# Kernel tuning notes

Measured on AMD Instinct MI355X. Metric: run time of the kernel, lower is better.

## Reference

```python
import jax, jax.numpy as jnp
import numpy as np

B, R, E, H = 1024, 1024, 1024, 512
L_ATTR, L_OBJ, L_RELA = 16, 36, 64
EPS = 1e-8


def _lstm_cell(x, h, c, Wih, Whh, bih, bhh):
    # torch.nn.LSTMCell: gates ordered i, f, g, o
    g = x @ Wih.T + bih + h @ Whh.T + bhh
    i, f, gg, o = jnp.split(g, 4, axis=1)
    c2 = jax.nn.sigmoid(f) * c + jax.nn.sigmoid(i) * jnp.tanh(gg)
    h2 = jax.nn.sigmoid(o) * jnp.tanh(c2)
    return h2, c2


def _attend(h, feats, p_feats, mask, Wq, bq, wa, ba):
    att_h = h @ Wq.T + bq                         # [B,H]
    dot = jnp.tanh(p_feats + att_h[:, None, :])   # [B,L,H]
    scores = dot @ wa + ba                        # [B,L]
    w = jax.nn.softmax(scores, axis=1)
    w = w * mask
    w = w / (w.sum(1, keepdims=True) + EPS)
    return jnp.einsum('bl,bld->bd', w, feats)     # [B,R]


def setup_inputs() -> dict:
    key = jax.random.key(0)
    ks = iter(jax.random.split(key, 64))
    n = lambda shp, s=0.02: jax.random.normal(next(ks), shp, dtype=jnp.float32) * s
    inp = {
        'xt': n((B, E), 1.0), 'fc_feats': n((B, R), 1.0),
        'state_h': n((2, B, R), 1.0), 'state_c': n((2, B, R), 1.0),
        'attr_feats': n((B, L_ATTR, R), 1.0), 'obj_feats': n((B, L_OBJ, R), 1.0),
        'rela_feats': n((B, L_RELA, R), 1.0),
        'p_attr_feats': n((B, L_ATTR, H), 1.0), 'p_obj_feats': n((B, L_OBJ, H), 1.0),
        'p_rela_feats': n((B, L_RELA, H), 1.0),
        'attr_masks': jnp.ones((B, L_ATTR), jnp.float32),
        'att_masks': jnp.ones((B, L_OBJ), jnp.float32),
        'rela_masks': jnp.ones((B, L_RELA), jnp.float32),
        'att_Wih': n((4 * R, E + 2 * R)), 'att_Whh': n((4 * R, R)),
        'att_bih': n((4 * R,)), 'att_bhh': n((4 * R,)),
        'lang_Wih': n((4 * R, 4 * R)), 'lang_Whh': n((4 * R, R)),
        'lang_bih': n((4 * R,)), 'lang_bhh': n((4 * R,)),
    }
    for p in ('attr', 'obj', 'rela'):
        inp[p + '_Wq'] = n((H, R)); inp[p + '_bq'] = n((H,))
        inp[p + '_wa'] = n((H,));   inp[p + '_ba'] = n((1,))
    return inp


def reference(xt, fc_feats, state_h, state_c, attr_feats, obj_feats, rela_feats,
              p_attr_feats, p_obj_feats, p_rela_feats, attr_masks, att_masks,
              rela_masks, att_Wih, att_Whh, att_bih, att_bhh, lang_Wih, lang_Whh,
              lang_bih, lang_bhh, attr_Wq, attr_bq, attr_wa, attr_ba, obj_Wq,
              obj_bq, obj_wa, obj_ba, rela_Wq, rela_bq, rela_wa, rela_ba):
    prev_h = state_h[-1]
    att_in = jnp.concatenate([prev_h, fc_feats, xt], axis=1)
    h_att, c_att = _lstm_cell(att_in, state_h[0], state_c[0],
                              att_Wih, att_Whh, att_bih, att_bhh)
    a_attr = _attend(h_att, attr_feats, p_attr_feats, attr_masks,
                     attr_Wq, attr_bq, attr_wa, attr_ba)
    a_obj = _attend(h_att, obj_feats, p_obj_feats, att_masks,
                    obj_Wq, obj_bq, obj_wa, obj_ba)
    a_rela = _attend(h_att, rela_feats, p_rela_feats, rela_masks,
                     rela_Wq, rela_bq, rela_wa, rela_ba)
    lang_in = jnp.concatenate([h_att, a_attr, a_obj, a_rela], axis=1)
    h_lang, c_lang = _lstm_cell(lang_in, state_h[1], state_c[1],
                                lang_Wih, lang_Whh, lang_bih, lang_bhh)
    # dropout in eval mode -> identity
    output = h_lang
    return output, jnp.stack([h_att, h_lang]), jnp.stack([c_att, c_lang])
```

## Files before the change

kernel.cpp:

```cpp
#include <hip/hip_runtime.h>
#include <math.h>

typedef _Float16 half8  __attribute__((ext_vector_type(8)));
typedef _Float16 half4v __attribute__((ext_vector_type(4)));
typedef float    f32x4  __attribute__((ext_vector_type(4)));

__device__ __forceinline__ _Float16 f2h(float f) { return (_Float16)f; }

__device__ __forceinline__ float tanh_fast(float x) {
    float e = __expf(2.f * x);
    return 1.f - 2.f / (e + 1.f);
}

#define LDSB (128 * 40)

__device__ __forceinline__ void gemm_body(
    _Float16* __restrict__ sm,
    const float* A0, const float* A1, const float* A2p, const float* A3,
    const float* A4,
    const float* W0, const float* W1, const float* W2,
    int w0cols, int w0s, int w1s, int nsel,
    _Float16* __restrict__ Cpart, int ldc,
    int kb, int kLen, int ntile, int mtile, int zout)
{
    _Float16* smA = sm;
    _Float16* smW = sm + 2 * LDSB;
    const int tid  = threadIdx.x;
    const int lane = tid & 63;
    const int wid  = tid >> 6;
    const int wm   = wid >> 1, wn = wid & 1;
    const int m0   = mtile * 128;
    const int n0   = ntile * 128;
    const int nt   = kLen >> 5;
    const int srow = tid >> 3;
    const int scol = (tid & 7) << 2;
    const int fr   = lane & 15;
    const int kq   = lane >> 4;

    const float* wsel = nullptr;
    if (nsel) {
        int sel = n0 >> 9;
        const float* Wq = (sel == 0) ? W0 : (sel == 1) ? W1 : W2;
        wsel = Wq + (size_t)((n0 & 511) + srow) * 1024 + kb + scol;
    }

    f32x4 acc[4][4] = {};
    float4 va[4], vw[4];

    auto LOADA = [&](int lk) {
        int gk = kb + lk;
        int seg = gk >> 10;
        const float* ap = (seg == 0) ? A0 : (seg == 1) ? A1 : (seg == 2) ? A2p
                        : (seg == 3) ? A3 : A4;
        ap += (size_t)(m0 + srow) * 1024 + (gk & 1023) + scol;
        #pragma unroll
        for (int p = 0; p < 4; ++p)
            va[p] = *reinterpret_cast<const float4*>(ap + (size_t)p * 32 * 1024);
    };
    auto LOADW = [&](int lk) {
        const float* wp; int wstr;
        if (nsel) {
            wp = wsel + lk; wstr = 1024;
        } else {
            int gk = kb + lk;
            if (gk < w0cols) { wp = W0 + (size_t)(n0 + srow) * w0s + gk + scol;            wstr = w0s; }
            else             { wp = W1 + (size_t)(n0 + srow) * w1s + (gk - w0cols) + scol; wstr = w1s; }
        }
        #pragma unroll
        for (int p = 0; p < 4; ++p)
            vw[p] = *reinterpret_cast<const float4*>(wp + (size_t)p * 32 * wstr);
    };
    auto WRITEA = [&](int buf) {
        _Float16* d = smA + buf * LDSB;
        #pragma unroll
        for (int p = 0; p < 4; ++p) {
            half4v h = { f2h(va[p].x), f2h(va[p].y), f2h(va[p].z), f2h(va[p].w) };
            *reinterpret_cast<half4v*>(&d[(srow + p * 32) * 40 + scol]) = h;
        }
    };
    auto WRITEW = [&](int buf) {
        _Float16* d = smW + buf * LDSB;
        #pragma unroll
        for (int p = 0; p < 4; ++p) {
            half4v h = { f2h(vw[p].x), f2h(vw[p].y), f2h(vw[p].z), f2h(vw[p].w) };
            *reinterpret_cast<half4v*>(&d[(srow + p * 32) * 40 + scol]) = h;
        }
    };
    auto DOMFMA = [&](int buf) {
        half8 af[4], bf[4];
        _Float16* sA = smA + buf * LDSB;
        _Float16* sW = smW + buf * LDSB;
        #pragma unroll
        for (int i = 0; i < 4; ++i) {
            af[i] = *reinterpret_cast<const half8*>(&sA[(wm * 64 + i * 16 + fr) * 40 + kq * 8]);
            bf[i] = *reinterpret_cast<const half8*>(&sW[(wn * 64 + i * 16 + fr) * 40 + kq * 8]);
        }
        #pragma unroll
        for (int i = 0; i < 4; ++i)
            #pragma unroll
            for (int j = 0; j < 4; ++j)
                acc[i][j] = __builtin_amdgcn_mfma_f32_16x16x32_f16(af[i], bf[j], acc[i][j], 0, 0, 0);
    };

    LOADA(0); LOADW(0);
    WRITEA(0); WRITEW(0);
    __syncthreads();
    int cur = 0;
    for (int it = 0; it < nt - 1; ++it) {
        LOADA((it + 1) * 32);
        LOADW((it + 1) * 32);
        DOMFMA(cur);
        WRITEA(cur ^ 1);
        WRITEW(cur ^ 1);
        __syncthreads();
        cur ^= 1;
    }
    DOMFMA(cur);

    _Float16* cp = Cpart + (size_t)zout * 1024ull * (size_t)ldc;
    #pragma unroll
    for (int j = 0; j < 4; ++j) {
        int nc = n0 + wn * 64 + j * 16 + fr;
        #pragma unroll
        for (int i = 0; i < 4; ++i) {
            int rb = m0 + wm * 64 + i * 16 + kq * 4;
            #pragma unroll
            for (int r = 0; r < 4; ++r)
                cp[(size_t)(rb + r) * ldc + nc] = (_Float16)acc[i][j][r];
        }
    }
}

__global__ __launch_bounds__(256) void gemm_hf(
    const float* A0, const float* A1, const float* A2p, const float* A3,
    const float* A4,
    const float* W0, const float* W1, const float* W2,
    int w0cols, int w0s, int w1s, int nsel,
    _Float16* Cpart, int ldc, int kLen, int zbase)
{
    __shared__ _Float16 sm[4 * LDSB];
    gemm_body(sm, A0, A1, A2p, A3, A4, W0, W1, W2, w0cols, w0s, w1s, nsel,
              Cpart, ldc, blockIdx.z * kLen, kLen,
              blockIdx.x, blockIdx.y, zbase + blockIdx.z);
}

__global__ __launch_bounds__(256) void gemm_hf_swz(
    const float* A0, const float* A1, const float* A2p, const float* A3,
    const float* A4,
    const float* W0, const float* W1, const float* W2,
    int w0cols, int w0s, int w1s,
    _Float16* Cpart, int ldc, int kLen, int zsplit)
{
    __shared__ _Float16 sm[4 * LDSB];
    const int bid = blockIdx.x;
    const int xcd = bid & 7;
    const int j   = bid >> 3;
    const int grp = xcd * (zsplit * 4) + (j >> 3);
    const int mtile = j & 7;
    const int ntile = grp / zsplit;
    const int z     = grp % zsplit;
    gemm_body(sm, A0, A1, A2p, A3, A4, W0, W1, W2, w0cols, w0s, w1s, 0,
              Cpart, ldc, z * kLen, kLen, ntile, mtile, z);
}


__global__ __launch_bounds__(256) void att_scores(
    const float* __restrict__ p_attr, const float* __restrict__ p_obj,
    const float* __restrict__ p_rela,
    const _Float16* __restrict__ q16,
    const float* __restrict__ attr_bq, const float* __restrict__ obj_bq,
    const float* __restrict__ rela_bq,
    const float* __restrict__ attr_wa, const float* __restrict__ obj_wa,
    const float* __restrict__ rela_wa,
    const float* __restrict__ attr_ba, const float* __restrict__ obj_ba,
    const float* __restrict__ rela_ba,
    float* __restrict__ scg)
{
    const unsigned gw = blockIdx.x * 4u + (threadIdx.x >> 6);
    const int lane = threadIdx.x & 63;
    const unsigned b = gw / 116u;
    const int r = (int)(gw - b * 116u);
    const float* pf; const float* bq; const float* wa; const float* ba;
    int l, moff, scoff, L;
    if (r < 16)      { pf = p_attr; bq = attr_bq; wa = attr_wa; ba = attr_ba; l = r;      moff = 0;    scoff = 0;  L = 16; }
    else if (r < 52) { pf = p_obj;  bq = obj_bq;  wa = obj_wa;  ba = obj_ba;  l = r - 16; moff = 512;  scoff = 16; L = 36; }
    else             { pf = p_rela; bq = rela_bq; wa = rela_wa; ba = rela_ba; l = r - 52; moff = 1024; scoff = 52; L = 64; }

    const float4* pf4 = reinterpret_cast<const float4*>(pf) + ((size_t)b * L + l) * 128 + lane * 2;
    float4 a0 = pf4[0];
    float4 a1 = pf4[1];
    const _Float16* qb = q16 + (size_t)b * 1536 + moff + lane * 8;
    half8 hq0 = *reinterpret_cast<const half8*>(qb);
    half8 hq1 = *reinterpret_cast<const half8*>(qb + 1536ull * 1024);
    const float4* bq4 = reinterpret_cast<const float4*>(bq) + lane * 2;
    const float4* wa4 = reinterpret_cast<const float4*>(wa) + lane * 2;
    float4 b0 = bq4[0], b1 = bq4[1];
    float4 w0 = wa4[0], w1 = wa4[1];

    float s = tanh_fast(a0.x + (float)hq0[0] + (float)hq1[0] + b0.x) * w0.x
            + tanh_fast(a0.y + (float)hq0[1] + (float)hq1[1] + b0.y) * w0.y
            + tanh_fast(a0.z + (float)hq0[2] + (float)hq1[2] + b0.z) * w0.z
            + tanh_fast(a0.w + (float)hq0[3] + (float)hq1[3] + b0.w) * w0.w
            + tanh_fast(a1.x + (float)hq0[4] + (float)hq1[4] + b1.x) * w1.x
            + tanh_fast(a1.y + (float)hq0[5] + (float)hq1[5] + b1.y) * w1.y
            + tanh_fast(a1.z + (float)hq0[6] + (float)hq1[6] + b1.z) * w1.z
            + tanh_fast(a1.w + (float)hq0[7] + (float)hq1[7] + b1.w) * w1.w;
    #pragma unroll
    for (int off = 32; off >= 1; off >>= 1) s += __shfl_xor(s, off);
    if (lane == 0) scg[(size_t)b * 128 + scoff + l] = s + ba[0];
}

template<int L>
__device__ __forceinline__ void wsum_mod(
    const float* __restrict__ feats, const float* __restrict__ scg_b,
    const float* __restrict__ mask_b,
    float* __restrict__ outa, int b, float* wgt)
{
    const int tid = threadIdx.x;
    if (tid < 64) {
        float v = (tid < L) ? scg_b[tid] : -1e30f;
        float m = v;
        #pragma unroll
        for (int off = 32; off >= 1; off >>= 1) m = fmaxf(m, __shfl_xor(m, off));
        float e = (tid < L) ? __expf(v - m) : 0.f;
        float sum = e;
        #pragma unroll
        for (int off = 32; off >= 1; off >>= 1) sum += __shfl_xor(sum, off);
        float w = e / sum;
        float wm = (tid < L) ? w * mask_b[tid] : 0.f;
        float s2 = wm;
        #pragma unroll
        for (int off = 32; off >= 1; off >>= 1) s2 += __shfl_xor(s2, off);
        wgt[tid] = wm / (s2 + 1e-8f);
    }
    __syncthreads();

    const int d0 = tid * 4;
    const float* fp = feats + (size_t)b * L * 1024 + d0;
    f32x4 acc = {0.f, 0.f, 0.f, 0.f};
    constexpr int NFULL = L / 8;
    float4 vA[8], vB[8];
    #pragma unroll
    for (int j = 0; j < 8; ++j)
        vA[j] = *reinterpret_cast<const float4*>(fp + (size_t)j * 1024);
    #pragma unroll
    for (int g = 0; g < NFULL; ++g) {
        float4* cur = (g & 1) ? vB : vA;
        float4* nxt = (g & 1) ? vA : vB;
        if (g + 1 < NFULL) {
            #pragma unroll
            for (int j = 0; j < 8; ++j)
                nxt[j] = *reinterpret_cast<const float4*>(fp + (size_t)((g + 1) * 8 + j) * 1024);
        }
        #pragma unroll
        for (int j = 0; j < 8; ++j) {
            const float w = wgt[g * 8 + j];
            acc[0] += w * cur[j].x; acc[1] += w * cur[j].y;
            acc[2] += w * cur[j].z; acc[3] += w * cur[j].w;
        }
    }
    #pragma unroll
    for (int lg = NFULL * 8; lg < L; ++lg) {
        float4 v = *reinterpret_cast<const float4*>(fp + (size_t)lg * 1024);
        const float w = wgt[lg];
        acc[0] += w * v.x; acc[1] += w * v.y; acc[2] += w * v.z; acc[3] += w * v.w;
    }
    float4 o; o.x = acc[0]; o.y = acc[1]; o.z = acc[2]; o.w = acc[3];
    *reinterpret_cast<float4*>(outa + (size_t)b * 1024 + d0) = o;
}

__global__ __launch_bounds__(256) void att_wsum(
    const float* __restrict__ attr_feats, const float* __restrict__ obj_feats,
    const float* __restrict__ rela_feats,
    const float* __restrict__ attr_masks, const float* __restrict__ att_masks,
    const float* __restrict__ rela_masks,
    const float* __restrict__ scg,
    float* __restrict__ a32)
{
    __shared__ float wgt[64];
    const int bid = blockIdx.x;
    const int mod = bid % 3;
    const int b   = bid / 3;
    if (mod == 0)
        wsum_mod<16>(attr_feats, scg + (size_t)b * 128 + 0,  attr_masks + (size_t)b * 16,
                     a32, b, wgt);
    else if (mod == 1)
        wsum_mod<36>(obj_feats,  scg + (size_t)b * 128 + 16, att_masks + (size_t)b * 36,
                     a32 + 1024ull * 1024, b, wgt);
    else
        wsum_mod<64>(rela_feats, scg + (size_t)b * 128 + 52, rela_masks + (size_t)b * 64,
                     a32 + 2ull * 1024 * 1024, b, wgt);
}

__global__ __launch_bounds__(256) void lstm4(
    const _Float16* __restrict__ g, size_t zstride, int nz,
    const float* __restrict__ bih, const float* __restrict__ bhh,
    const float* __restrict__ c_prev,
    float* __restrict__ hA, float* __restrict__ hB,
    float* __restrict__ c_out)
{
    int idx = blockIdx.x * 256 + threadIdx.x;
    int b = idx >> 10, r = idx & 1023;
    size_t base = (size_t)b * 4096;
    float gi = bih[r]        + bhh[r];
    float gf = bih[1024 + r] + bhh[1024 + r];
    float gg = bih[2048 + r] + bhh[2048 + r];
    float go = bih[3072 + r] + bhh[3072 + r];
    for (int z = 0; z < nz; ++z) {
        const _Float16* gz = g + (size_t)z * zstride + base;
        gi += (float)gz[r];
        gf += (float)gz[1024 + r];
        gg += (float)gz[2048 + r];
        go += (float)gz[3072 + r];
    }
    float si = 1.f / (1.f + __expf(-gi));
    float sf = 1.f / (1.f + __expf(-gf));
    float so = 1.f / (1.f + __expf(-go));
    float c2 = sf * c_prev[idx] + si * tanh_fast(gg);
    float h2 = so * tanh_fast(c2);
    hA[idx] = h2;
    if (hB) hB[idx] = h2;
    c_out[idx] = c2;
}

extern "C" void kernel_launch(void* const* d_in, const int* in_sizes, int n_in,
                              void* d_out, int out_size, void* d_ws, size_t ws_size,
                              hipStream_t stream)
{
    const size_t BR = 1024ull * 1024ull;
    const float* xt         = (const float*)d_in[0];
    const float* fc         = (const float*)d_in[1];
    const float* state_h    = (const float*)d_in[2];
    const float* state_c    = (const float*)d_in[3];
    const float* attr_feats = (const float*)d_in[4];
    const float* obj_feats  = (const float*)d_in[5];
    const float* rela_feats = (const float*)d_in[6];
    const float* p_attr     = (const float*)d_in[7];
    const float* p_obj      = (const float*)d_in[8];
    const float* p_rela     = (const float*)d_in[9];
    const float* attr_masks = (const float*)d_in[10];
    const float* att_masks  = (const float*)d_in[11];
    const float* rela_masks = (const float*)d_in[12];
    const float* att_Wih    = (const float*)d_in[13];
    const float* att_Whh    = (const float*)d_in[14];
    const float* att_bih    = (const float*)d_in[15];
    const float* att_bhh    = (const float*)d_in[16];
    const float* lang_Wih   = (const float*)d_in[17];
    const float* lang_Whh   = (const float*)d_in[18];
    const float* lang_bih   = (const float*)d_in[19];
    const float* lang_bhh   = (const float*)d_in[20];
    const float* attr_Wq    = (const float*)d_in[21];
    const float* attr_bq    = (const float*)d_in[22];
    const float* attr_wa    = (const float*)d_in[23];
    const float* attr_ba    = (const float*)d_in[24];
    const float* obj_Wq     = (const float*)d_in[25];
    const float* obj_bq     = (const float*)d_in[26];
    const float* obj_wa     = (const float*)d_in[27];
    const float* obj_ba     = (const float*)d_in[28];
    const float* rela_Wq    = (const float*)d_in[29];
    const float* rela_bq    = (const float*)d_in[30];
    const float* rela_wa    = (const float*)d_in[31];
    const float* rela_ba    = (const float*)d_in[32];

    float* out = (float*)d_out;
    const float* h0 = state_h;
    const float* h1 = state_h + BR;
    float* h_att = out + BR;
    float* scg  = out;

    const bool big = ws_size >= 52428800ull;
    const int gslots = big ? 4 : 2;
    _Float16* g16 = (_Float16*)d_ws;
    _Float16* q16 = g16 + (size_t)gslots * 4ull * BR;
    float*    a32 = (float*)(q16 + 2ull * 1536 * 1024);
    float* a_attr = a32;
    float* a_obj  = a32 + BR;
    float* a_rela = a32 + 2 * BR;

    dim3 blk(256);
    const int zsplit = big ? 4 : 2;

    gemm_hf_swz<<<dim3(256 * zsplit), blk, 0, stream>>>(
        h1, fc, xt, h0, h0, att_Wih, att_Whh, att_Whh,
        3072, 3072, 1024, g16, 4096, 4096 / zsplit, zsplit);
    lstm4<<<dim3(4096), blk, 0, stream>>>(
        g16, 4ull * BR, gslots, att_bih, att_bhh, state_c,
        h_att, nullptr, out + 3 * BR);
    gemm_hf<<<dim3(12, 8, 2), blk, 0, stream>>>(
        h_att, h_att, h_att, h_att, h_att,
        attr_Wq, obj_Wq, rela_Wq, 0, 1024, 1024, 1,
        q16, 1536, 512, 0);
    att_scores<<<dim3(29696), blk, 0, stream>>>(
        p_attr, p_obj, p_rela, q16,
        attr_bq, obj_bq, rela_bq, attr_wa, obj_wa, rela_wa,
        attr_ba, obj_ba, rela_ba, scg);
    att_wsum<<<dim3(3072), blk, 0, stream>>>(
        attr_feats, obj_feats, rela_feats,
        attr_masks, att_masks, rela_masks, scg, a32);
    gemm_hf_swz<<<dim3(256 * zsplit), blk, 0, stream>>>(
        h_att, a_attr, a_obj, a_rela, h1,
        lang_Wih, lang_Whh, lang_Whh, 4096, 4096, 1024,
        g16, 4096, 5120 / zsplit, zsplit);
    lstm4<<<dim3(4096), blk, 0, stream>>>(
        g16, 4ull * BR, gslots, lang_bih, lang_bhh, state_c + BR,
        out, out + 2 * BR, out + 4 * BR);
}
```

Baseline: 428.8 us.

## Replace split-K LSTM GEMMs with 512-thread 256x128 tiled double-buffered kernel

The two large LSTM gate GEMMs now run through a new 512-thread kernel using 256x128 output tiles, with register-staged fp32-to-fp16 conversion into double-buffered LDS and 16x16x32 MFMAs. It also uses a new XCD-aware block-to-tile mapping. Larger tiles raise arithmetic intensity and cut redundant reads of A and W, at the cost of fewer blocks, higher register and LDS use, and uncoalesced fp16 stores. The attention weighted-sum loop also drops explicit double-buffering in favour of straight loads with two accumulators.

```diff
diff --git a/kernel.cpp b/kernel.cpp
--- a/kernel.cpp
+++ b/kernel.cpp
@@ -144,25 +144,121 @@
               blockIdx.x, blockIdx.y, zbase + blockIdx.z);
 }
 
-__global__ __launch_bounds__(256) void gemm_hf_swz(
+__global__ __launch_bounds__(512) void gemm512(
     const float* A0, const float* A1, const float* A2p, const float* A3,
     const float* A4,
     const float* W0, const float* W1, const float* W2,
     int w0cols, int w0s, int w1s,
     _Float16* Cpart, int ldc, int kLen, int zsplit)
 {
-    __shared__ _Float16 sm[4 * LDSB];
+    __shared__ _Float16 smA[2][256 * 40];
+    __shared__ _Float16 smW[2][128 * 40];
+    const int perXcd = (4 * zsplit) >> 3;
     const int bid = blockIdx.x;
     const int xcd = bid & 7;
     const int j   = bid >> 3;
-    const int grp = xcd * (zsplit * 4) + (j >> 3);
-    const int mtile = j & 7;
-    const int ntile = grp / zsplit;
+    const int grp = xcd * perXcd + (j >> 5);
+    const int ntile = j & 31;
+    const int mtile = grp / zsplit;
     const int z     = grp % zsplit;
-    gemm_body(sm, A0, A1, A2p, A3, A4, W0, W1, W2, w0cols, w0s, w1s, 0,
-              Cpart, ldc, z * kLen, kLen, ntile, mtile, z);
-}
-
+    const int kb    = z * kLen;
+    const int m0    = mtile * 256;
+    const int n0    = ntile * 128;
+    const int nt    = kLen >> 5;
+
+    const int tid  = threadIdx.x;
+    const int lane = tid & 63;
+    const int wid  = tid >> 6;
+    const int wm   = wid >> 1;
+    const int wn   = wid & 1;
+    const int fr   = lane & 15;
+    const int kq   = lane >> 4;
+
+    const int arow = tid >> 1;
+    const int acol = (tid & 1) << 4;
+    const int wrow = tid >> 2;
+    const int wcol = (tid & 3) << 3;
+
+    f32x4 acc[4][4] = {};
+    float4 va[4], vw[2];
+
+    auto LOADA = [&](int lk) {
+        int gk = kb + lk;
+        int seg = gk >> 10;
+        const float* ap = (seg == 0) ? A0 : (seg == 1) ? A1 : (seg == 2) ? A2p
+                        : (seg == 3) ? A3 : A4;
+        ap += (size_t)(m0 + arow) * 1024 + (gk & 1023) + acol;
+        #pragma unroll
+        for (int p = 0; p < 4; ++p)
+            va[p] = *reinterpret_cast<const float4*>(ap + p * 4);
+    };
+    auto LOADW = [&](int lk) {
+        int gk = kb + lk;
+        const float* wp; int wstr;
+        if (gk < w0cols) { wp = W0 + (size_t)(n0 + wrow) * w0s + gk + wcol;            wstr = w0s; }
+        else             { wp = W1 + (size_t)(n0 + wrow) * w1s + (gk - w0cols) + wcol; wstr = w1s; }
+        (void)wstr;
+        #pragma unroll
+        for (int p = 0; p < 2; ++p)
+            vw[p] = *reinterpret_cast<const float4*>(wp + p * 4);
+    };
+    auto WRITEA = [&](int buf) {
+        _Float16* d = &smA[buf][arow * 40 + acol];
+        half8 h0 = { f2h(va[0].x), f2h(va[0].y), f2h(va[0].z), f2h(va[0].w),
+                     f2h(va[1].x), f2h(va[1].y), f2h(va[1].z), f2h(va[1].w) };
+        half8 h1 = { f2h(va[2].x), f2h(va[2].y), f2h(va[2].z), f2h(va[2].w),
+                     f2h(va[3].x), f2h(va[3].y), f2h(va[3].z), f2h(va[3].w) };
+        *reinterpret_cast<half8*>(d)     = h0;
+        *reinterpret_cast<half8*>(d + 8) = h1;
+    };
+    auto WRITEW = [&](int buf) {
+        _Float16* d = &smW[buf][wrow * 40 + wcol];
+        half8 h0 = { f2h(vw[0].x), f2h(vw[0].y), f2h(vw[0].z), f2h(vw[0].w),
+                     f2h(vw[1].x), f2h(vw[1].y), f2h(vw[1].z), f2h(vw[1].w) };
+        *reinterpret_cast<half8*>(d) = h0;
+    };
+    auto DOMFMA = [&](int buf) {
+        half8 af[4], bf[4];
+        #pragma unroll
+        for (int i = 0; i < 4; ++i) {
+            af[i] = *reinterpret_cast<const half8*>(&smA[buf][(wm * 64 + i * 16 + fr) * 40 + kq * 8]);
+            bf[i] = *reinterpret_cast<const half8*>(&smW[buf][(wn * 64 + i * 16 + fr) * 40 + kq * 8]);
+        }
+        #pragma unroll
+        for (int i = 0; i < 4; ++i)
+            #pragma unroll
+            for (int jj = 0; jj < 4; ++jj)
+                acc[i][jj] = __builtin_amdgcn_mfma_f32_16x16x32_f16(af[i], bf[jj], acc[i][jj], 0, 0, 0);
+    };
+
+    LOADA(0); LOADW(0);
+    WRITEA(0); WRITEW(0);
+    __syncthreads();
+    int cur = 0;
+    for (int it = 0; it < nt - 1; ++it) {
+        LOADA((it + 1) * 32);
+        LOADW((it + 1) * 32);
+        DOMFMA(cur);
+        WRITEA(cur ^ 1);
+        WRITEW(cur ^ 1);
+        __syncthreads();
+        cur ^= 1;
+    }
+    DOMFMA(cur);
+
+    _Float16* cp = Cpart + (size_t)z * 1024ull * (size_t)ldc;
+    #pragma unroll
+    for (int jj = 0; jj < 4; ++jj) {
+        int nc = n0 + wn * 64 + jj * 16 + fr;
+        #pragma unroll
+        for (int i = 0; i < 4; ++i) {
+            int rb = m0 + wm * 64 + i * 16 + kq * 4;
+            #pragma unroll
+            for (int r = 0; r < 4; ++r)
+                cp[(size_t)(rb + r) * ldc + nc] = (_Float16)acc[i][jj][r];
+        }
+    }
+}
 
 __global__ __launch_bounds__(256) void att_scores(
     const float* __restrict__ p_attr, const float* __restrict__ p_obj,
@@ -237,35 +333,41 @@
 
     const int d0 = tid * 4;
     const float* fp = feats + (size_t)b * L * 1024 + d0;
-    f32x4 acc = {0.f, 0.f, 0.f, 0.f};
+    f32x4 acc0 = {0.f, 0.f, 0.f, 0.f};
+    f32x4 acc1 = {0.f, 0.f, 0.f, 0.f};
     constexpr int NFULL = L / 8;
-    float4 vA[8], vB[8];
-    #pragma unroll
-    for (int j = 0; j < 8; ++j)
-        vA[j] = *reinterpret_cast<const float4*>(fp + (size_t)j * 1024);
     #pragma unroll
     for (int g = 0; g < NFULL; ++g) {
-        float4* cur = (g & 1) ? vB : vA;
-        float4* nxt = (g & 1) ? vA : vB;
-        if (g + 1 < NFULL) {
-            #pragma unroll
-            for (int j = 0; j < 8; ++j)
-                nxt[j] = *reinterpret_cast<const float4*>(fp + (size_t)((g + 1) * 8 + j) * 1024);
-        }
-        #pragma unroll
-        for (int j = 0; j < 8; ++j) {
-            const float w = wgt[g * 8 + j];
-            acc[0] += w * cur[j].x; acc[1] += w * cur[j].y;
-            acc[2] += w * cur[j].z; acc[3] += w * cur[j].w;
-        }
+        float4 v0 = *reinterpret_cast<const float4*>(fp + (size_t)(g * 8 + 0) * 1024);
+        float4 v1 = *reinterpret_cast<const float4*>(fp + (size_t)(g * 8 + 1) * 1024);
+        float4 v2 = *reinterpret_cast<const float4*>(fp + (size_t)(g * 8 + 2) * 1024);
+        float4 v3 = *reinterpret_cast<const float4*>(fp + (size_t)(g * 8 + 3) * 1024);
+        float4 v4 = *reinterpret_cast<const float4*>(fp + (size_t)(g * 8 + 4) * 1024);
+        float4 v5 = *reinterpret_cast<const float4*>(fp + (size_t)(g * 8 + 5) * 1024);
+        float4 v6 = *reinterpret_cast<const float4*>(fp + (size_t)(g * 8 + 6) * 1024);
+        float4 v7 = *reinterpret_cast<const float4*>(fp + (size_t)(g * 8 + 7) * 1024);
+        float w0 = wgt[g * 8 + 0], w1 = wgt[g * 8 + 1], w2 = wgt[g * 8 + 2], w3 = wgt[g * 8 + 3];
+        float w4 = wgt[g * 8 + 4], w5 = wgt[g * 8 + 5], w6 = wgt[g * 8 + 6], w7 = wgt[g * 8 + 7];
+        acc0[0] += w0 * v0.x + w2 * v2.x + w4 * v4.x + w6 * v6.x;
+        acc0[1] += w0 * v0.y + w2 * v2.y + w4 * v4.y + w6 * v6.y;
+        acc0[2] += w0 * v0.z + w2 * v2.z + w4 * v4.z + w6 * v6.z;
+        acc0[3] += w0 * v0.w + w2 * v2.w + w4 * v4.w + w6 * v6.w;
+        acc1[0] += w1 * v1.x + w3 * v3.x + w5 * v5.x + w7 * v7.x;
+        acc1[1] += w1 * v1.y + w3 * v3.y + w5 * v5.y + w7 * v7.y;
+        acc1[2] += w1 * v1.z + w3 * v3.z + w5 * v5.z + w7 * v7.z;
+        acc1[3] += w1 * v1.w + w3 * v3.w + w5 * v5.w + w7 * v7.w;
     }
     #pragma unroll
-    for (int lg = NFULL * 8; lg < L; ++lg) {
-        float4 v = *reinterpret_cast<const float4*>(fp + (size_t)lg * 1024);
-        const float w = wgt[lg];
-        acc[0] += w * v.x; acc[1] += w * v.y; acc[2] += w * v.z; acc[3] += w * v.w;
-    }
-    float4 o; o.x = acc[0]; o.y = acc[1]; o.z = acc[2]; o.w = acc[3];
+    for (int lg = NFULL * 8; lg < L; lg += 2) {
+        float4 v0 = *reinterpret_cast<const float4*>(fp + (size_t)lg * 1024);
+        float4 v1 = *reinterpret_cast<const float4*>(fp + (size_t)(lg + 1) * 1024);
+        float w0 = wgt[lg], w1 = wgt[lg + 1];
+        acc0[0] += w0 * v0.x; acc0[1] += w0 * v0.y; acc0[2] += w0 * v0.z; acc0[3] += w0 * v0.w;
+        acc1[0] += w1 * v1.x; acc1[1] += w1 * v1.y; acc1[2] += w1 * v1.z; acc1[3] += w1 * v1.w;
+    }
+    float4 o;
+    o.x = acc0[0] + acc1[0]; o.y = acc0[1] + acc1[1];
+    o.z = acc0[2] + acc1[2]; o.w = acc0[3] + acc1[3];
     *reinterpret_cast<float4*>(outa + (size_t)b * 1024 + d0) = o;
 }
 
@@ -379,8 +481,9 @@
 
     dim3 blk(256);
     const int zsplit = big ? 4 : 2;
-
-    gemm_hf_swz<<<dim3(256 * zsplit), blk, 0, stream>>>(
+    const int gemmGrid = 256 * ((4 * zsplit) >> 3);
+
+    gemm512<<<dim3(gemmGrid), dim3(512), 0, stream>>>(
         h1, fc, xt, h0, h0, att_Wih, att_Whh, att_Whh,
         3072, 3072, 1024, g16, 4096, 4096 / zsplit, zsplit);
     lstm4<<<dim3(4096), blk, 0, stream>>>(
@@ -397,7 +500,7 @@
     att_wsum<<<dim3(3072), blk, 0, stream>>>(
         attr_feats, obj_feats, rela_feats,
         attr_masks, att_masks, rela_masks, scg, a32);
-    gemm_hf_swz<<<dim3(256 * zsplit), blk, 0, stream>>>(
+    gemm512<<<dim3(gemmGrid), dim3(512), 0, stream>>>(
         h_att, a_attr, a_obj, a_rela, h1,
         lang_Wih, lang_Whh, lang_Whh, 4096, 4096, 1024,
         g16, 4096, 5120 / zsplit, zsplit);
```

Result: slower. 461.5 us (+7.6%).
